# Performance work log

Hardware: AMD Instinct MI355X
Metric: run time of the kernel (lower is better)

The kernel has to match this reference:

```python
import jax, jax.numpy as jnp
import numpy as np

D = 512
MOMENTUM = 0.99
NEG_INF = -1.0e9


def setup_inputs() -> dict:
    key = jax.random.key(0)
    ks = jax.random.split(key, 16)
    B, Lq, Lk = 16, 1024, 1024
    s = 0.02
    inp = {
        "uncond_q": jax.random.normal(ks[0], (B, D), jnp.float32),
        "q": jax.random.normal(ks[1], (B, Lq, D), jnp.float32),
        "k": jax.random.normal(ks[2], (B, Lk, D), jnp.float32),
        "v": jax.random.normal(ks[3], (B, Lk, D), jnp.float32),
        "src_key_padding_mask": jax.random.randint(ks[4], (B, Lk), 0, 2) > 0,
        "fallback_score": jnp.zeros((1,), jnp.float32),
        # parameters (torch Linear: y = x @ W.T + b)
        "Wv": jax.random.normal(ks[5], (D, D), jnp.float32) * s,
        "bv": jnp.zeros((D,), jnp.float32),
        "Wf": jax.random.normal(ks[6], (D, D), jnp.float32) * s,
        "bf": jnp.zeros((D,), jnp.float32),
        "W1": jax.random.normal(ks[7], (D, D), jnp.float32) * s,
        "b1": jnp.zeros((D,), jnp.float32),
        "W2": jax.random.normal(ks[8], (D // 2, D), jnp.float32) * s,
        "b2": jnp.zeros((D // 2,), jnp.float32),
        "W3": jax.random.normal(ks[9], (1, D // 2), jnp.float32) * s,
        "b3": jnp.zeros((1,), jnp.float32),
    }
    return inp


def _scorer(x, W1, b1, W2, b2, W3, b3):
    h = jax.nn.relu(x @ W1.T + b1)
    h = jax.nn.relu(h @ W2.T + b2)
    return jnp.tanh(h @ W3.T + b3)


def reference(uncond_q, q, k, v, src_key_padding_mask, fallback_score,
              Wv, bv, Wf, bf, W1, b1, W2, b2, W3, b3):
    B, Lq, _ = q.shape
    v_p = v @ Wv.T + bv                                  # [B,Lk,D]
    default_values = (uncond_q @ Wf.T + bf)[:, None, :]  # [B,1,D]

    scores = jnp.einsum('bqd,bkd->bqk', q, k) / jnp.sqrt(jnp.float32(D))

    # EMA fallback-score update (training mode), detached from grads
    bmax = jax.lax.stop_gradient(scores.max())
    bmin = jax.lax.stop_gradient(scores.min())
    fb = MOMENTUM * fallback_score[0] + (1.0 - MOMENTUM) * (bmax + bmin) / 2.0

    scores = jnp.where(src_key_padding_mask[:, None, :], NEG_INF, scores)
    fb_col = jnp.broadcast_to(fb, (B, Lq, 1))
    scores = jnp.concatenate([scores, fb_col], axis=-1)   # [B,Lq,Lk+1]
    weights = jax.nn.softmax(scores, axis=-1)

    v_padded = jnp.concatenate([v_p, default_values], axis=1)  # [B,Lk+1,D]
    out = jnp.einsum('bqk,bkd->bqd', weights, v_padded)

    return (_scorer(out, W1, b1, W2, b2, W3, b3),
            _scorer(default_values, W1, b1, W2, b2, W3, b3))
```

## Files before the change

### kernel.cpp

```cpp
#include <hip/hip_runtime.h>

typedef _Float16 f16;
typedef f16  f16x8 __attribute__((ext_vector_type(8)));
typedef f16  f16x4 __attribute__((ext_vector_type(4)));
typedef __fp16 fp16x2 __attribute__((ext_vector_type(2)));
typedef float f32x4 __attribute__((ext_vector_type(4)));

__device__ __forceinline__ void gld_lds16(const f16* g, void* l) {
  __builtin_amdgcn_global_load_lds((const __attribute__((address_space(1))) void*)g,
                                   (__attribute__((address_space(3))) void*)l,
                                   16, 0, 0);
}
__device__ __forceinline__ void gld_lds16f(const float* g, void* l) {
  __builtin_amdgcn_global_load_lds((const __attribute__((address_space(1))) void*)g,
                                   (__attribute__((address_space(3))) void*)l,
                                   16, 0, 0);
}

__device__ __forceinline__ f16x8 pack8(float4 a, float4 b) {
  union { f16x8 v; fp16x2 h[4]; } u;
  u.h[0] = __builtin_amdgcn_cvt_pkrtz(a.x, a.y);
  u.h[1] = __builtin_amdgcn_cvt_pkrtz(a.z, a.w);
  u.h[2] = __builtin_amdgcn_cvt_pkrtz(b.x, b.y);
  u.h[3] = __builtin_amdgcn_cvt_pkrtz(b.z, b.w);
  return u.v;
}

enum { EPI_SCORES = 0, EPI_RELU = 2, EPI_OUT = 3, EPI_BIASR = 4 };

template<int EPI, bool XMAP>
__global__ __launch_bounds__(256)
void gemm_bt(const f16* __restrict__ A, const f16* __restrict__ B, void* __restrict__ C,
             int lda, int ldb, int ldc, int K,
             long long sA, long long sB, long long sC,
             const float* __restrict__ bias, float scale,
             float* __restrict__ mmarr, int nmm,
             const float* __restrict__ wfb, const float* __restrict__ dvv,
             int nx, int nbz)
{
  __shared__ __align__(16) f16 As[3][128][32];
  __shared__ __align__(16) f16 Bs[3][128][32];
  const int tid  = threadIdx.x;
  const int lane = tid & 63;
  const int w    = tid >> 6;
  const int wm   = w >> 1, wn = w & 1;

  const int lin = blockIdx.x;
  int bz, bj;
  if constexpr (XMAP) {
    const int xcd = lin & 7, rest = lin >> 3;
    const int grp = rest / nbz;
    bj = rest - grp * nbz;
    bz = xcd + (grp << 3);
  } else {
    bz = lin / nbz; bj = lin - bz * nbz;
  }
  const int m0 = (bj / nx) * 128, n0 = (bj % nx) * 128;
  const f16* Ab = A + (size_t)bz * sA + (size_t)m0 * lda;
  const f16* Bb = B + (size_t)bz * sB + (size_t)n0 * ldb;

  f32x4 acc[4][4] = {};
  const int nsteps = K >> 5;

#define STAGE(bufb, ks)                                                              \
  {                                                                                  \
    const int k0_ = (ks) << 5;                                                       \
    _Pragma("unroll")                                                                \
    for (int i = 0; i < 2; ++i) {                                                    \
      const int ci = i * 256 + tid;                                                  \
      const int r  = ci >> 2;                                                        \
      const int sg = (ci & 3) ^ ((r >> 1) & 3);                                      \
      gld_lds16(Ab + (size_t)r * lda + k0_ + sg * 8,                                 \
                (char*)As + (bufb) + (size_t)(i * 256 + w * 64) * 16);               \
      gld_lds16(Bb + (size_t)r * ldb + k0_ + sg * 8,                                 \
                (char*)Bs + (bufb) + (size_t)(i * 256 + w * 64) * 16);               \
    }                                                                                \
  }

  STAGE(0, 0)
  STAGE(8192, 1)

  const int elemoff = (((lane >> 4) ^ ((lane >> 1) & 3)) << 3);

  int cur = 0;
  for (int t = 0; t < nsteps; ++t) {
    if (t + 1 < nsteps) asm volatile("s_waitcnt vmcnt(4)" ::: "memory");
    else                asm volatile("s_waitcnt vmcnt(0)" ::: "memory");
    __builtin_amdgcn_s_barrier();
    __builtin_amdgcn_sched_barrier(0);
    int st = cur + 2; if (st >= 3) st -= 3;
    if (t + 2 < nsteps) STAGE(st * 8192, t + 2)
    f16x8 af[4], bfr[4];
#pragma unroll
    for (int m = 0; m < 4; ++m)
      af[m] = *(const f16x8*)&As[cur][wm * 64 + m * 16 + (lane & 15)][elemoff];
#pragma unroll
    for (int n = 0; n < 4; ++n)
      bfr[n] = *(const f16x8*)&Bs[cur][wn * 64 + n * 16 + (lane & 15)][elemoff];
    __builtin_amdgcn_s_setprio(1);
#pragma unroll
    for (int m = 0; m < 4; ++m)
#pragma unroll
      for (int n = 0; n < 4; ++n)
        acc[m][n] = __builtin_amdgcn_mfma_f32_16x16x32_f16(af[m], bfr[n], acc[m][n], 0, 0, 0);
    __builtin_amdgcn_s_setprio(0);
    cur = (cur + 1 == 3) ? 0 : cur + 1;
  }
#undef STAGE

  const int col_l = lane & 15;
  const int row_l = (lane >> 4) << 2;

  {
    f16* Ch = (f16*)C + (size_t)bz * sC + (size_t)m0 * ldc + n0;
#pragma unroll
    for (int m = 0; m < 4; ++m)
#pragma unroll
      for (int n = 0; n < 4; ++n)
#pragma unroll
        for (int r = 0; r < 4; ++r) {
          const int rr = wm * 64 + m * 16 + row_l + r;
          const int cc = wn * 64 + n * 16 + col_l;
          float val = acc[m][n][r];
          if constexpr (EPI == EPI_RELU) { val += bias[n0 + cc]; val = fmaxf(val, 0.0f); }
          if constexpr (EPI == EPI_BIASR) val += bias[m0 + rr];
          if constexpr (EPI == EPI_OUT)
            val += wfb[bz * 1024 + m0 + rr] * dvv[bz * 512 + n0 + cc];
          Ch[(size_t)rr * ldc + cc] = (f16)val;
        }
  }
  (void)scale; (void)mmarr; (void)nmm;
}

__global__ __launch_bounds__(512, 2)
void gemm256_scores(const float* __restrict__ A, const float* __restrict__ B, f16* __restrict__ C,
                    float scale, float* __restrict__ mmarr)
{
  __shared__ __align__(16) float AsF[2][256][32];
  __shared__ __align__(16) float BsF[2][256][32];
  __shared__ float redm[8], redn[8];
  const int tid  = threadIdx.x;
  const int lane = tid & 63;
  const int w    = tid >> 6;
  const int wm   = w >> 2, wn = w & 3;
  const int lin  = blockIdx.x;
  const int xcd = lin & 7, rest = lin >> 3;
  const int bj  = rest & 15;
  const int bz  = xcd + ((rest >> 4) << 3);
  const int m0 = (bj >> 2) * 256, n0 = (bj & 3) * 256;
  const float* Ab = A + (size_t)bz * 524288 + (size_t)m0 * 512;
  const float* Bb = B + (size_t)bz * 524288 + (size_t)n0 * 512;

  f32x4 acc[8][4] = {};

#define STAGEF(bufb, ks)                                                             \
  {                                                                                  \
    const int k0_ = (ks) << 5;                                                       \
    _Pragma("unroll")                                                                \
    for (int i = 0; i < 4; ++i) {                                                    \
      const int ci = i * 512 + tid;                                                  \
      const int r  = ci >> 3;                                                        \
      const int sg = (ci & 7) ^ (((ci >> 4) & 3) << 1);                              \
      gld_lds16f(Ab + (size_t)r * 512 + k0_ + sg * 4,                                \
                 (char*)AsF + (bufb) + (size_t)ci * 16);                             \
      gld_lds16f(Bb + (size_t)r * 512 + k0_ + sg * 4,                                \
                 (char*)BsF + (bufb) + (size_t)ci * 16);                             \
    }                                                                                \
  }

  STAGEF(0, 0)
  STAGEF(32768, 1)

  const int fr = lane & 15;
  const int eo = (((lane >> 4) ^ ((lane >> 1) & 3)) << 3);

  int cur = 0;
  for (int t = 0; t < 16; ++t) {
    if (t < 15) asm volatile("s_waitcnt vmcnt(8)" ::: "memory");
    else        asm volatile("s_waitcnt vmcnt(0)" ::: "memory");
    __builtin_amdgcn_s_barrier();
    __builtin_amdgcn_sched_barrier(0);
    const float* Ac = (const float*)((const char*)AsF + cur * 32768);
    const float* Bc = (const float*)((const char*)BsF + cur * 32768);
    f16x8 af[8], bfr[4];
#pragma unroll
    for (int m = 0; m < 8; ++m) {
      const float* p = Ac + (size_t)(wm * 128 + m * 16 + fr) * 32 + eo;
      af[m] = pack8(*(const float4*)p, *(const float4*)(p + 4));
    }
#pragma unroll
    for (int n = 0; n < 4; ++n) {
      const float* p = Bc + (size_t)(wn * 64 + n * 16 + fr) * 32 + eo;
      bfr[n] = pack8(*(const float4*)p, *(const float4*)(p + 4));
    }
    __builtin_amdgcn_s_setprio(1);
#pragma unroll
    for (int m = 0; m < 8; ++m)
#pragma unroll
      for (int n = 0; n < 4; ++n)
        acc[m][n] = __builtin_amdgcn_mfma_f32_16x16x32_f16(af[m], bfr[n], acc[m][n], 0, 0, 0);
    __builtin_amdgcn_s_setprio(0);
    __builtin_amdgcn_s_barrier();
    if (t + 2 < 16) STAGEF(cur * 32768, t + 2)
    cur ^= 1;
  }
#undef STAGEF

  const int col_l = lane & 15;
  const int row_l = (lane >> 4) << 2;
  f16* Ch = C + (size_t)bz * 1048576 + (size_t)m0 * 1024 + n0;
  float lmax = -3.402823466e38f, lmin = 3.402823466e38f;
#pragma unroll
  for (int m = 0; m < 8; ++m)
#pragma unroll
    for (int n = 0; n < 4; ++n)
#pragma unroll
      for (int r = 0; r < 4; ++r) {
        float val = acc[m][n][r] * scale;
        lmax = fmaxf(lmax, val); lmin = fminf(lmin, val);
        Ch[(size_t)(wm * 128 + m * 16 + row_l + r) * 1024 + (wn * 64 + n * 16 + col_l)] = (f16)val;
      }
#pragma unroll
  for (int off = 32; off >= 1; off >>= 1) {
    lmax = fmaxf(lmax, __shfl_xor(lmax, off));
    lmin = fminf(lmin, __shfl_xor(lmin, off));
  }
  if (lane == 0) { redm[w] = lmax; redn[w] = lmin; }
  __syncthreads();
  if (tid == 0) {
    float gm = redm[0], gn = redn[0];
#pragma unroll
    for (int i = 1; i < 8; ++i) { gm = fmaxf(gm, redm[i]); gn = fminf(gn, redn[i]); }
    mmarr[lin] = gm; mmarr[256 + lin] = gn;
  }
}

__global__ __launch_bounds__(256)
void reduce_mm(const float* __restrict__ mmarr, int n,
               const float* __restrict__ fallback, float* __restrict__ fbv,
               const unsigned char* __restrict__ mask, unsigned* __restrict__ mm)
{
  __shared__ float rm[4], rn[4];
  __shared__ int redc[256];
  const int lane = threadIdx.x & 63, w = threadIdx.x >> 6;
  float mx = -3.402823466e38f, mn = 3.402823466e38f;
  for (int i = threadIdx.x; i < n; i += 256) {
    mx = fmaxf(mx, mmarr[i]);
    mn = fminf(mn, mmarr[n + i]);
  }
#pragma unroll
  for (int off = 32; off >= 1; off >>= 1) {
    mx = fmaxf(mx, __shfl_xor(mx, off));
    mn = fminf(mn, __shfl_xor(mn, off));
  }
  if (lane == 0) { rm[w] = mx; rn[w] = mn; }
  int c = 0;
  for (int i = threadIdx.x; i < 16384; i += 256) c += (mask[i] != 0) ? 1 : 0;
  redc[threadIdx.x] = c;
  __syncthreads();
  for (int s = 128; s > 0; s >>= 1) {
    if (threadIdx.x < s) redc[threadIdx.x] += redc[threadIdx.x + s];
    __syncthreads();
  }
  if (threadIdx.x == 0) {
    float gmax = fmaxf(fmaxf(rm[0], rm[1]), fmaxf(rm[2], rm[3]));
    float gmin = fminf(fminf(rn[0], rn[1]), fminf(rn[2], rn[3]));
    fbv[0] = 0.99f * fallback[0] + 0.005f * (gmax + gmin);
    mm[0] = (unsigned)redc[0];
  }
}

__global__ __launch_bounds__(256)
void conv_v(const float* __restrict__ v, f16* __restrict__ v16)
{
  const int i = blockIdx.x * 256 + threadIdx.x;
#pragma unroll
  for (int it = 0; it < 4; ++it) {
    const size_t j = (size_t)i + (size_t)it * 524288;
    float4 x = *(const float4*)(v + j * 4);
    f16x4 o = { (f16)x.x, (f16)x.y, (f16)x.z, (f16)x.w };
    *(f16x4*)(v16 + j * 4) = o;
  }
}

__global__ __launch_bounds__(256)
void convw_k(const float* __restrict__ wv, const float* __restrict__ w1,
             const float* __restrict__ w2,
             f16* __restrict__ owv, f16* __restrict__ ow1, f16* __restrict__ ow2)
{
  int i = blockIdx.x * 256 + threadIdx.x;
  const float* src; f16* dst; int j;
  if (i < 65536)       { src = wv; dst = owv; j = i; }
  else if (i < 131072) { src = w1; dst = ow1; j = i - 65536; }
  else                 { src = w2; dst = ow2; j = i - 131072; }
  float4 v = *(const float4*)(src + (size_t)j * 4);
  f16x4 o = { (f16)v.x, (f16)v.y, (f16)v.z, (f16)v.w };
  *(f16x4*)(dst + (size_t)j * 4) = o;
}

__global__ __launch_bounds__(256)
void softmax_rows(const f16* __restrict__ scores, const void* __restrict__ maskp,
                  const float* __restrict__ fbv, const unsigned* __restrict__ mm,
                  f16* __restrict__ Wt, float* __restrict__ wfb)
{
  __shared__ float red[8];
  const int row  = blockIdx.x;
  const int b    = row >> 10;
  const int tid  = threadIdx.x;
  const int lane = tid & 63, w = tid >> 6;
  const float fb = fbv[0];
  const unsigned mode = (mm[0] > 5000u) ? 1u : 0u;
  const f16* s = scores + (size_t)row * 1024;
  const int k0 = tid * 4;
  f16x4 sv = *(const f16x4*)(s + k0);
  float x[4];
  if (mode) {
    const unsigned char* m8 = (const unsigned char*)maskp + b * 1024 + k0;
    x[0] = m8[0] ? -1e9f : (float)sv[0];  x[1] = m8[1] ? -1e9f : (float)sv[1];
    x[2] = m8[2] ? -1e9f : (float)sv[2];  x[3] = m8[3] ? -1e9f : (float)sv[3];
  } else {
    const int* mi = (const int*)maskp + b * 1024 + k0;
    x[0] = mi[0] ? -1e9f : (float)sv[0];  x[1] = mi[1] ? -1e9f : (float)sv[1];
    x[2] = mi[2] ? -1e9f : (float)sv[2];  x[3] = mi[3] ? -1e9f : (float)sv[3];
  }
  float mx = fmaxf(fmaxf(x[0], x[1]), fmaxf(x[2], x[3]));
#pragma unroll
  for (int off = 32; off >= 1; off >>= 1) mx = fmaxf(mx, __shfl_xor(mx, off));
  if (lane == 0) red[w] = mx;
  __syncthreads();
  mx = fmaxf(fmaxf(fmaxf(red[0], red[1]), fmaxf(red[2], red[3])), fb);
  float e0 = expf(x[0] - mx), e1 = expf(x[1] - mx), e2 = expf(x[2] - mx), e3 = expf(x[3] - mx);
  float sum = (e0 + e1) + (e2 + e3);
#pragma unroll
  for (int off = 32; off >= 1; off >>= 1) sum += __shfl_xor(sum, off);
  if (lane == 0) red[4 + w] = sum;
  __syncthreads();
  float efb = expf(fb - mx);
  float Z = ((red[4] + red[5]) + (red[6] + red[7])) + efb;
  float inv = 1.0f / Z;
  f16x4 o = { (f16)(e0 * inv), (f16)(e1 * inv), (f16)(e2 * inv), (f16)(e3 * inv) };
  *(f16x4*)&Wt[(size_t)row * 1024 + k0] = o;
  if (tid == 0) wfb[row] = efb * inv;
}

template<int IN, int ACT>
__global__ __launch_bounds__(256)
void fc_wave(const float* __restrict__ X, const float* __restrict__ W,
             const float* __restrict__ bias, float* __restrict__ Y, int OutN)
{
  const int gw   = (blockIdx.x * 256 + threadIdx.x) >> 6;
  const int lane = threadIdx.x & 63;
  const int b = gw / OutN, j = gw - b * OutN;
  const float* x  = X + (size_t)b * IN;
  const float* wr = W + (size_t)j * IN;
  float s = 0.f;
  if constexpr (IN == 512) {
    const int o = lane * 8;
    float4 x0 = *(const float4*)(x + o),  x1 = *(const float4*)(x + o + 4);
    float4 w0 = *(const float4*)(wr + o), w1 = *(const float4*)(wr + o + 4);
    s = x0.x*w0.x + x0.y*w0.y + x0.z*w0.z + x0.w*w0.w
      + x1.x*w1.x + x1.y*w1.y + x1.z*w1.z + x1.w*w1.w;
  } else {
    const int o = lane * 4;
    float4 x0 = *(const float4*)(x + o);
    float4 w0 = *(const float4*)(wr + o);
    s = x0.x*w0.x + x0.y*w0.y + x0.z*w0.z + x0.w*w0.w;
  }
#pragma unroll
  for (int off = 32; off >= 1; off >>= 1) s += __shfl_xor(s, off);
  if (lane == 0) {
    float val = s + bias[ACT == 2 ? 0 : j];
    if constexpr (ACT == 1) val = fmaxf(val, 0.f);
    if constexpr (ACT == 2) val = tanhf(val);
    Y[gw] = val;
  }
}

__global__ __launch_bounds__(256)
void y_kernel(const f16* __restrict__ h2, const float* __restrict__ W3,
              const float* __restrict__ b3, float* __restrict__ outp)
{
  int row = blockIdx.x * 16 + (threadIdx.x >> 4);
  int l   = threadIdx.x & 15;
  const f16* h = h2 + (size_t)row * 256 + l * 16;
  float s = 0.f;
#pragma unroll
  for (int j = 0; j < 16; ++j) s += (float)h[j] * W3[l * 16 + j];
#pragma unroll
  for (int off = 1; off < 16; off <<= 1) s += __shfl_xor(s, off);
  if (l == 0) outp[row] = tanhf(s + b3[0]);
}

extern "C" void kernel_launch(void* const* d_in, const int* in_sizes, int n_in,
                              void* d_out, int out_size, void* d_ws, size_t ws_size,
                              hipStream_t stream) {
  const float* uq       = (const float*)d_in[0];
  const float* q        = (const float*)d_in[1];
  const float* kk       = (const float*)d_in[2];
  const float* v        = (const float*)d_in[3];
  const void*  mask     = d_in[4];
  const float* fallback = (const float*)d_in[5];
  const float* Wv = (const float*)d_in[6];
  const float* bv = (const float*)d_in[7];
  const float* Wf = (const float*)d_in[8];
  const float* bf = (const float*)d_in[9];
  const float* W1 = (const float*)d_in[10];
  const float* b1 = (const float*)d_in[11];
  const float* W2 = (const float*)d_in[12];
  const float* b2 = (const float*)d_in[13];
  const float* W3 = (const float*)d_in[14];
  const float* b3 = (const float*)d_in[15];
  float* outp = (float*)d_out;

  char* ws = (char*)d_ws;
  const size_t MB = 1ull << 20;
  f16*  scores = (f16*)ws;
  f16*  h1b  = (f16*)ws;
  f16*  h2b  = (f16*)(ws + 16 * MB);
  f16*  vpt  = (f16*)(ws + 32 * MB);
  f16*  outb = (f16*)(ws + 48 * MB);
  f16*  wts  = (f16*)(ws + 64 * MB);
  f16*  v16  = (f16*)(ws + 96 * MB);
  char* cst  = ws + 112 * MB;
  f16*  Wv16 = (f16*)(cst);
  f16*  W116 = (f16*)(cst + 512 * 1024);
  f16*  W216 = (f16*)(cst + 1024 * 1024);
  float* dv   = (float*)(cst + 1280 * 1024);
  float* wfb  = (float*)(cst + 1312 * 1024);
  float* h1d  = (float*)(cst + 1376 * 1024);
  float* h2d  = (float*)(cst + 1408 * 1024);
  unsigned* mm = (unsigned*)(cst + 1424 * 1024);
  float* fbv   = (float*)(cst + 1428 * 1024);
  float* mmarr = (float*)(cst + 1432 * 1024);

  conv_v<<<2048, 256, 0, stream>>>(v, v16);
  convw_k<<<640, 256, 0, stream>>>(Wv, W1, W2, Wv16, W116, W216);

  fc_wave<512, 0><<<2048, 256, 0, stream>>>(uq, Wf, bf, dv, 512);

  gemm256_scores<<<256, 512, 0, stream>>>(q, kk, scores, 0.04419417382415922f, mmarr);

  reduce_mm<<<1, 256, 0, stream>>>(mmarr, 256, fallback, fbv,
                                   (const unsigned char*)mask, mm);

  softmax_rows<<<16384, 256, 0, stream>>>(scores, mask, fbv, mm, wts, wfb);

  gemm_bt<EPI_BIASR, true><<<512, 256, 0, stream>>>(
      Wv16, v16, vpt, 512, 512, 1024, 512,
      0LL, 524288LL, 524288LL,
      bv, 1.f, nullptr, 0, nullptr, nullptr, 8, 32);

  gemm_bt<EPI_OUT, true><<<512, 256, 0, stream>>>(
      wts, vpt, outb, 1024, 1024, 512, 1024,
      1048576LL, 524288LL, 524288LL,
      nullptr, 1.f, nullptr, 0, wfb, dv, 4, 32);

  gemm_bt<EPI_RELU, false><<<512, 256, 0, stream>>>(
      outb, W116, h1b, 512, 512, 512, 512, 0LL, 0LL, 0LL,
      b1, 1.f, nullptr, 0, nullptr, nullptr, 4, 512);

  gemm_bt<EPI_RELU, false><<<256, 256, 0, stream>>>(
      h1b, W216, h2b, 512, 512, 256, 512, 0LL, 0LL, 0LL,
      b2, 1.f, nullptr, 0, nullptr, nullptr, 2, 256);

  y_kernel<<<1024, 256, 0, stream>>>(h2b, W3, b3, outp);

  fc_wave<512, 1><<<2048, 256, 0, stream>>>(dv, W1, b1, h1d, 512);
  fc_wave<512, 1><<<1024, 256, 0, stream>>>(h1d, W2, b2, h2d, 256);
  fc_wave<256, 2><<<4, 256, 0, stream>>>(h2d, W3, b3, outp + 16384, 1);

  (void)in_sizes; (void)n_in; (void)out_size; (void)ws_size;
}
```

Measured before the change: 175.1 us.

## Deepen gemm_bt LDS pipeline to four stages and merge front-end kernels

The gemm_bt kernel moves from a 3-buffer to a 4-buffer LDS ring, prefetching three k-steps ahead with matching vmcnt waits, to hide more global-load latency. This doubles-ish LDS use (64KB per block), which may lower occupancy. Separately, the v conversion, weight conversion and default-value FC kernels are merged into one launch (front_k) to cut launch overhead and let them run concurrently.

Measured after the change: 169.7 us. -3.1%, faster.

```diff
diff --git a/kernel.cpp b/kernel.cpp
--- a/kernel.cpp
+++ b/kernel.cpp
@@ -38,8 +38,8 @@
              const float* __restrict__ wfb, const float* __restrict__ dvv,
              int nx, int nbz)
 {
-  __shared__ __align__(16) f16 As[3][128][32];
-  __shared__ __align__(16) f16 Bs[3][128][32];
+  __shared__ __align__(16) f16 As[4][128][32];
+  __shared__ __align__(16) f16 Bs[4][128][32];
   const int tid  = threadIdx.x;
   const int lane = tid & 63;
   const int w    = tid >> 6;
@@ -78,18 +78,19 @@
   }
 
   STAGE(0, 0)
-  STAGE(8192, 1)
+  if (1 < nsteps) STAGE(8192, 1)
+  if (2 < nsteps) STAGE(16384, 2)
 
   const int elemoff = (((lane >> 4) ^ ((lane >> 1) & 3)) << 3);
 
   int cur = 0;
   for (int t = 0; t < nsteps; ++t) {
-    if (t + 1 < nsteps) asm volatile("s_waitcnt vmcnt(4)" ::: "memory");
-    else                asm volatile("s_waitcnt vmcnt(0)" ::: "memory");
+    if (t + 2 < nsteps)      asm volatile("s_waitcnt vmcnt(8)" ::: "memory");
+    else if (t + 1 < nsteps) asm volatile("s_waitcnt vmcnt(4)" ::: "memory");
+    else                     asm volatile("s_waitcnt vmcnt(0)" ::: "memory");
     __builtin_amdgcn_s_barrier();
     __builtin_amdgcn_sched_barrier(0);
-    int st = cur + 2; if (st >= 3) st -= 3;
-    if (t + 2 < nsteps) STAGE(st * 8192, t + 2)
+    if (t + 3 < nsteps) STAGE(((cur + 3) & 3) * 8192, t + 3)
     f16x8 af[4], bfr[4];
 #pragma unroll
     for (int m = 0; m < 4; ++m)
@@ -104,7 +105,7 @@
       for (int n = 0; n < 4; ++n)
         acc[m][n] = __builtin_amdgcn_mfma_f32_16x16x32_f16(af[m], bfr[n], acc[m][n], 0, 0, 0);
     __builtin_amdgcn_s_setprio(0);
-    cur = (cur + 1 == 3) ? 0 : cur + 1;
+    cur = (cur + 1) & 3;
   }
 #undef STAGE
 
@@ -271,31 +272,47 @@
 }
 
 __global__ __launch_bounds__(256)
-void conv_v(const float* __restrict__ v, f16* __restrict__ v16)
-{
-  const int i = blockIdx.x * 256 + threadIdx.x;
-#pragma unroll
-  for (int it = 0; it < 4; ++it) {
-    const size_t j = (size_t)i + (size_t)it * 524288;
-    float4 x = *(const float4*)(v + j * 4);
+void front_k(const float* __restrict__ v, f16* __restrict__ v16,
+             const float* __restrict__ wv, const float* __restrict__ w1,
+             const float* __restrict__ w2,
+             f16* __restrict__ owv, f16* __restrict__ ow1, f16* __restrict__ ow2,
+             const float* __restrict__ uq, const float* __restrict__ Wf,
+             const float* __restrict__ bfv, float* __restrict__ dv)
+{
+  const int blk = blockIdx.x;
+  if (blk < 2048) {
+    const int i = blk * 256 + threadIdx.x;
+#pragma unroll
+    for (int it = 0; it < 4; ++it) {
+      const size_t j = (size_t)i + (size_t)it * 524288;
+      float4 x = *(const float4*)(v + j * 4);
+      f16x4 o = { (f16)x.x, (f16)x.y, (f16)x.z, (f16)x.w };
+      *(f16x4*)(v16 + j * 4) = o;
+    }
+  } else if (blk < 2688) {
+    int i = (blk - 2048) * 256 + threadIdx.x;
+    const float* src; f16* dst; int j;
+    if (i < 65536)       { src = wv; dst = owv; j = i; }
+    else if (i < 131072) { src = w1; dst = ow1; j = i - 65536; }
+    else                 { src = w2; dst = ow2; j = i - 131072; }
+    float4 x = *(const float4*)(src + (size_t)j * 4);
     f16x4 o = { (f16)x.x, (f16)x.y, (f16)x.z, (f16)x.w };
-    *(f16x4*)(v16 + j * 4) = o;
-  }
-}
-
-__global__ __launch_bounds__(256)
-void convw_k(const float* __restrict__ wv, const float* __restrict__ w1,
-             const float* __restrict__ w2,
-             f16* __restrict__ owv, f16* __restrict__ ow1, f16* __restrict__ ow2)
-{
-  int i = blockIdx.x * 256 + threadIdx.x;
-  const float* src; f16* dst; int j;
-  if (i < 65536)       { src = wv; dst = owv; j = i; }
-  else if (i < 131072) { src = w1; dst = ow1; j = i - 65536; }
-  else                 { src = w2; dst = ow2; j = i - 131072; }
-  float4 v = *(const float4*)(src + (size_t)j * 4);
-  f16x4 o = { (f16)v.x, (f16)v.y, (f16)v.z, (f16)v.w };
-  *(f16x4*)(dst + (size_t)j * 4) = o;
+    *(f16x4*)(dst + (size_t)j * 4) = o;
+  } else {
+    const int gw   = ((blk - 2688) * 256 + threadIdx.x) >> 6;
+    const int lane = threadIdx.x & 63;
+    const int b = gw >> 9, j = gw & 511;
+    const float* x  = uq + (size_t)b * 512;
+    const float* wr = Wf + (size_t)j * 512;
+    const int o = lane * 8;
+    float4 x0 = *(const float4*)(x + o),  x1 = *(const float4*)(x + o + 4);
+    float4 w0 = *(const float4*)(wr + o), w1v = *(const float4*)(wr + o + 4);
+    float s = x0.x*w0.x + x0.y*w0.y + x0.z*w0.z + x0.w*w0.w
+            + x1.x*w1v.x + x1.y*w1v.y + x1.z*w1v.z + x1.w*w1v.w;
+#pragma unroll
+    for (int off = 32; off >= 1; off >>= 1) s += __shfl_xor(s, off);
+    if (lane == 0) dv[gw] = s + bfv[j];
+  }
 }
 
 __global__ __launch_bounds__(256)
@@ -433,10 +450,8 @@
   float* fbv   = (float*)(cst + 1428 * 1024);
   float* mmarr = (float*)(cst + 1432 * 1024);
 
-  conv_v<<<2048, 256, 0, stream>>>(v, v16);
-  convw_k<<<640, 256, 0, stream>>>(Wv, W1, W2, Wv16, W116, W216);
-
-  fc_wave<512, 0><<<2048, 256, 0, stream>>>(uq, Wf, bf, dv, 512);
+  front_k<<<4736, 256, 0, stream>>>(v, v16, Wv, W1, W2, Wv16, W116, W216,
+                                    uq, Wf, bf, dv);
 
   gemm256_scores<<<256, 512, 0, stream>>>(q, kk, scores, 0.04419417382415922f, mmarr);
 
```
